# Optimization experiments

Measured on AMD Instinct MI355X. Metric: run time of the kernel, lower is better.

The kernel has to match this reference:

```python
import jax, jax.numpy as jnp
import numpy as np

HID, DIN, ORDER = 64, 1, 2
EPS = 1e-5


def conv1x1(x, W, b):
    # x: [b, c_in, n] -> [b, c_out, n]
    return jnp.einsum('oi,bin->bon', W, x) + b[:, None]


def gconv(x, supports, W, b, order, include_self):
    outs = [x] if include_self else []
    for A in supports:
        x1 = jnp.einsum('bcv,wv->bcw', x, A)
        outs.append(x1)
        for _ in range(order - 1):
            x1 = jnp.einsum('bcv,wv->bcw', x1, A)
            outs.append(x1)
    return conv1x1(jnp.concatenate(outs, axis=1), W, b)


def _forward(x, mask, adj, h0, fs_W, fs_b, li_W, li_b, gc_W, gc_b, lo_W, lo_b,
             ro_W, ro_b, prelu_a, f_W, f_b, u_W, u_b, c_W, c_b, gn_g, gn_beta):
    B = x.shape[0]
    supports = [adj[0], adj[1]]
    h = jnp.broadcast_to(h0, (B,) + h0.shape)  # [b, HID, n]

    def step(h, inp):
        x_s, m_s = inp  # [b, DIN, n] each
        mbool = m_s > 0
        # first stage prediction from hidden state
        xs_hat_1 = conv1x1(h, fs_W, fs_b)
        x1 = jnp.where(mbool, x_s, xs_hat_1)
        # spatial decoder (order=1, no attention)
        x_in = conv1x1(jnp.concatenate([x1, m_s, h], axis=1), li_W, li_b)
        out = gconv(x_in, supports, gc_W, gc_b, order=1, include_self=False)
        out = conv1x1(jnp.concatenate([out, h], axis=1), lo_W, lo_b)
        out = jnp.where(out >= 0, out, prelu_a * out)  # PReLU
        repr_s = jnp.concatenate([out, h], axis=1)     # [b, 2*HID, n]
        xs_hat_2 = conv1x1(repr_s, ro_W, ro_b)
        x2 = jnp.where(mbool, x1, xs_hat_2)
        # GCGRU cell (order-2 graph conv gates, include_self=True)
        rnn_in = jnp.concatenate([x2, m_s], axis=1)    # [b, 2*DIN, n]
        xh = jnp.concatenate([rnn_in, h], axis=1)
        r = jax.nn.sigmoid(gconv(xh, supports, f_W, f_b, ORDER, True))
        u = jax.nn.sigmoid(gconv(xh, supports, u_W, u_b, ORDER, True))
        xc = jnp.concatenate([rnn_in, r * h], axis=1)
        c = jnp.tanh(gconv(xc, supports, c_W, c_b, ORDER, True))
        h_new = u * h + (1.0 - u) * c
        # GroupNorm(num_groups=1): normalize over (C, N) per sample
        mu = h_new.mean(axis=(1, 2), keepdims=True)
        var = h_new.var(axis=(1, 2), keepdims=True)
        h_n = (h_new - mu) / jnp.sqrt(var + EPS) * gn_g[:, None] + gn_beta[:, None]
        return h_n, (xs_hat_2, xs_hat_1, h_n, repr_s)

    xs = jnp.moveaxis(x, -1, 0)     # [T, b, DIN, n]
    ms = jnp.moveaxis(mask, -1, 0)
    _, (imp, pred, states, reprs) = jax.lax.scan(step, h, (xs, ms))
    imputations = jnp.moveaxis(imp, 0, -1)          # [b, DIN, n, T]
    predictions = jnp.moveaxis(pred, 0, -1)
    states = jnp.moveaxis(states, 0, -1)[None]      # [n_layers=1, b, HID, n, T]
    representations = jnp.moveaxis(reprs, 0, -1)    # [b, 2*HID, n, T]
    return imputations, predictions, representations, states


def setup_inputs() -> dict:
    key = jax.random.key(0)
    ks = jax.random.split(key, 24)
    B, N, T = 8, 1024, 24
    rnn_in = 2 * DIN                 # x + mask
    dec_in = rnn_in + HID            # 66
    gate_in = 5 * (rnn_in + HID)     # (order*support_len + self) * (d_in + hidden)

    def w(k, o, i):
        return (jax.random.normal(k, (o, i), jnp.float32) / np.sqrt(i)).astype(jnp.float32)

    x = jax.random.normal(ks[0], (B, DIN, N, T), jnp.float32)
    mask = jax.random.bernoulli(ks[1], 0.8, (B, DIN, N, T)).astype(jnp.float32)
    A = jax.random.uniform(ks[2], (N, N), jnp.float32)
    A = A * (A > 0.97)  # sparse-ish graph
    fwd = A / (A.sum(1, keepdims=True) + 1e-8)
    bwd = A.T / (A.T.sum(1, keepdims=True) + 1e-8)
    adj = jnp.stack([fwd, bwd])
    return {
        'x': x, 'mask': mask, 'adj': adj,
        'h0': jax.random.normal(ks[3], (HID, N), jnp.float32) / np.sqrt(HID),
        'fs_W': w(ks[4], DIN, HID), 'fs_b': jnp.zeros((DIN,), jnp.float32),
        'li_W': w(ks[5], HID, dec_in), 'li_b': jnp.zeros((HID,), jnp.float32),
        'gc_W': w(ks[6], HID, 2 * HID), 'gc_b': jnp.zeros((HID,), jnp.float32),
        'lo_W': w(ks[7], HID, 2 * HID), 'lo_b': jnp.zeros((HID,), jnp.float32),
        'ro_W': w(ks[8], DIN, 2 * HID), 'ro_b': jnp.zeros((DIN,), jnp.float32),
        'prelu_a': jnp.float32(0.25),
        'f_W': w(ks[9], HID, gate_in), 'f_b': jnp.zeros((HID,), jnp.float32),
        'u_W': w(ks[10], HID, gate_in), 'u_b': jnp.zeros((HID,), jnp.float32),
        'c_W': w(ks[11], HID, gate_in), 'c_b': jnp.zeros((HID,), jnp.float32),
        'gn_g': jnp.ones((HID,), jnp.float32), 'gn_beta': jnp.zeros((HID,), jnp.float32),
    }


def reference(x, mask, adj, h0, fs_W, fs_b, li_W, li_b, gc_W, gc_b, lo_W, lo_b,
              ro_W, ro_b, prelu_a, f_W, f_b, u_W, u_b, c_W, c_b, gn_g, gn_beta):
    return _forward(x, mask, adj, h0, fs_W, fs_b, li_W, li_b, gc_W, gc_b,
                    lo_W, lo_b, ro_W, ro_b, prelu_a, f_W, f_b, u_W, u_b,
                    c_W, c_b, gn_g, gn_beta)
```

## Files before the change

### kernel.cpp

```cpp
#include <hip/hip_runtime.h>
#include <hip/hip_bf16.h>

typedef __hip_bfloat16 bf16;

constexpr int NV=1024, TT=24, BB=8, CAP=80;

constexpr int O_CVAL = 0;
constexpr int O_CIDX = 163840;
constexpr int O_CCNT = 327680;
constexpr int O_LIWT = 329728;
constexpr int O_GCWT = 333952;
constexpr int O_LOWT = 342144;
constexpr int O_FWT  = 350336;
constexpr int O_UWT  = 371456;
constexpr int O_CWT  = 392576;
constexpr int O_H    = 413696;
constexpr int O_T1   = 937984;
constexpr int O_T3   = 1986560;
constexpr int O_XH   = 2510848;
constexpr int O_Z1F  = 3067904;
constexpr int O_Z1B  = 3624960;
constexpr int O_PART = 4182016;
constexpr int O_RST  = 5296144;
constexpr int O_SST  = 17879056;
constexpr size_t WS_FLOATS = 24170512;
constexpr int O_XC = O_T1;
constexpr int O_U  = O_T3;

constexpr int OFF_IMP  = 0;
constexpr int OFF_PRED = 196608;
constexpr int OFF_REPR = 393216;
constexpr int OFF_ST   = 25559040;

__device__ __forceinline__ bf16 f2b(float v){ return __float2bfloat16(v); }
__device__ __forceinline__ float b2f(bf16 v){ return __bfloat162float(v); }

__global__ __launch_bounds__(64) void k_csr(const float* __restrict__ adj, float* __restrict__ ws){
  int row = blockIdx.x, lane = threadIdx.x;
  const float* a = adj + (size_t)row*NV;
  float* val = ws + O_CVAL + (size_t)row*CAP;
  int* idx = (int*)(ws+O_CIDX) + (size_t)row*CAP;
  int count = 0;
  for(int ch=0; ch<NV/64; ++ch){
    float v = a[ch*64+lane];
    unsigned long long m = __ballot(v != 0.f);
    int pre = __popcll(m & ((1ull<<lane)-1ull));
    if(v != 0.f){ int p = count+pre; if(p<CAP){ idx[p]=ch*64+lane; val[p]=v; } }
    count += __popcll(m);
  }
  if(lane==0) ((int*)(ws+O_CCNT))[row] = count>CAP?CAP:count;
}

__global__ void k_prep_wt(const float* __restrict__ liW, const float* __restrict__ gcW,
    const float* __restrict__ loW, const float* __restrict__ fW,
    const float* __restrict__ uW, const float* __restrict__ cW, float* __restrict__ ws){
  int g = blockIdx.x*blockDim.x + threadIdx.x, G = gridDim.x*blockDim.x;
  for(int i=g;i<66*64;i+=G){ int k=i>>6, c=i&63; ws[O_LIWT+i]=liW[c*66+k]; }
  for(int i=g;i<128*64;i+=G){ int k=i>>6, c=i&63; ws[O_GCWT+i]=gcW[c*128+k]; ws[O_LOWT+i]=loW[c*128+k]; }
  for(int i=g;i<330*64;i+=G){ int k=i>>6, c=i&63; ws[O_FWT+i]=fW[c*330+k]; ws[O_UWT+i]=uW[c*330+k]; ws[O_CWT+i]=cW[c*330+k]; }
}

__global__ __launch_bounds__(256) void k_h0(const float* __restrict__ h0, float* __restrict__ ws){
  int g = blockIdx.x*blockDim.x + threadIdx.x;
  if(g >= BB*NV*64) return;
  int c = g&63, n = (g>>6)&1023;
  ws[O_H + g] = h0[c*NV + n];
}

__global__ __launch_bounds__(256) void kA(float* __restrict__ ws,
    const float* __restrict__ x, const float* __restrict__ mask,
    const float* __restrict__ fsW, const float* __restrict__ fsb,
    const float* __restrict__ lib, const float* __restrict__ gng,
    const float* __restrict__ gnb, float* __restrict__ dout, int t){
  __shared__ float hs[4][2][64];
  __shared__ float musd[8][2];
  int tid = threadIdx.x, wid = tid>>6, lane = tid&63;
  int n = blockIdx.x;
  if(t > 0){
    const float2* part = (const float2*)(ws+O_PART);
    int b = wid*2 + (lane>>5);
    int l5 = lane&31;
    float sx=0.f, sq=0.f;
    for(int i=l5;i<1024;i+=32){ float2 pp = part[b*1024+i]; sx+=pp.x; sq+=pp.y; }
    #pragma unroll
    for(int off=16;off;off>>=1){ sx+=__shfl_xor(sx,off,64); sq+=__shfl_xor(sq,off,64); }
    if(l5==0){ float mu=sx*(1.f/65536.f);
               musd[b][0]=mu; musd[b][1]=rsqrtf(sq*(1.f/65536.f)-mu*mu+1e-5f); }
    __syncthreads();
  }
  float gg = gng[lane], gb = gnb[lane];
  float x1v[2], xmv[2];
  #pragma unroll
  for(int j=0;j<2;++j){
    int b = wid*2+j;
    size_t col = (size_t)(b*NV+n);
    float h = ws[O_H + col*64 + lane];
    if(t > 0){
      h = (h - musd[b][0])*musd[b][1]*gg + gb;
      ws[O_H + col*64 + lane] = h;
      ((bf16*)(ws+O_SST))[(size_t)(t-1)*(BB*NV*64) + col*64 + lane] = f2b(h);
    }
    hs[wid][j][lane] = h;
    float pv = fsW[lane]*h;
    #pragma unroll
    for(int off=32; off; off>>=1) pv += __shfl_xor(pv, off, 64);
    float pred = pv + fsb[0];
    float xm = mask[col*TT + t];
    x1v[j] = (xm>0.f) ? x[col*TT + t] : pred;
    xmv[j] = xm;
    if(lane==0) dout[OFF_PRED + col*TT + t] = pred;
  }
  const float* Wt = ws + O_LIWT;
  float lb = lib[lane];
  float w0 = Wt[lane], w1 = Wt[64+lane];
  float a0 = lb + w0*x1v[0] + w1*xmv[0];
  float a1 = lb + w0*x1v[1] + w1*xmv[1];
  for(int j=0;j<64;++j){
    float w = Wt[(2+j)*64+lane];
    a0 += w*hs[wid][0][j];
    a1 += w*hs[wid][1][j];
  }
  ws[O_T1 + (size_t)((wid*2  )*NV+n)*64 + lane] = a0;
  ws[O_T1 + (size_t)((wid*2+1)*NV+n)*64 + lane] = a1;
}

__global__ __launch_bounds__(256) void kB(float* __restrict__ ws,
    const float* __restrict__ x, const float* __restrict__ mask,
    const float* __restrict__ gcb, const float* __restrict__ lob,
    const float* __restrict__ prelu, const float* __restrict__ roW,
    const float* __restrict__ rob, float* __restrict__ dout, int t){
  __shared__ float pq[4][2][128];
  int tid=threadIdx.x, wid=tid>>6, lane=tid&63;
  int n = blockIdx.x;
  int b0 = wid*2, b1 = wid*2+1;
  const int* ccnt = (const int*)(ws+O_CCNT);
  float p0=0.f,p1=0.f,q0=0.f,q1=0.f;
  {
    int cn = ccnt[n];
    const int* id = (const int*)(ws+O_CIDX) + (size_t)n*CAP;
    const float* vl = ws + O_CVAL + (size_t)n*CAP;
    #pragma unroll 4
    for(int k=0;k<cn;++k){
      float a = vl[k]; int ix = id[k];
      p0 += a*ws[O_T1 + (size_t)(b0*NV+ix)*64 + lane];
      p1 += a*ws[O_T1 + (size_t)(b1*NV+ix)*64 + lane];
    }
  }
  {
    int cn = ccnt[NV+n];
    const int* id = (const int*)(ws+O_CIDX) + (size_t)(NV+n)*CAP;
    const float* vl = ws + O_CVAL + (size_t)(NV+n)*CAP;
    #pragma unroll 4
    for(int k=0;k<cn;++k){
      float a = vl[k]; int ix = id[k];
      q0 += a*ws[O_T1 + (size_t)(b0*NV+ix)*64 + lane];
      q1 += a*ws[O_T1 + (size_t)(b1*NV+ix)*64 + lane];
    }
  }
  pq[wid][0][lane]=p0; pq[wid][0][64+lane]=q0;
  pq[wid][1][lane]=p1; pq[wid][1][64+lane]=q1;
  const float* Gt = ws + O_GCWT;
  float g0 = gcb[lane], g1 = g0;
  for(int j=0;j<128;++j){
    float w = Gt[j*64+lane];
    g0 += w*pq[wid][0][j];
    g1 += w*pq[wid][1][j];
  }
  float hv0 = ws[O_H + (size_t)(b0*NV+n)*64 + lane];
  float hv1 = ws[O_H + (size_t)(b1*NV+n)*64 + lane];
  pq[wid][0][lane]=g0; pq[wid][0][64+lane]=hv0;
  pq[wid][1][lane]=g1; pq[wid][1][64+lane]=hv1;
  const float* Lt = ws + O_LOWT;
  float o0 = lob[lane], o1 = o0;
  for(int j=0;j<128;++j){
    float w = Lt[j*64+lane];
    o0 += w*pq[wid][0][j];
    o1 += w*pq[wid][1][j];
  }
  float a = prelu[0];
  float r0 = roW[lane], r1 = roW[64+lane], rb0 = rob[0];
  bf16* reprs = (bf16*)(ws + O_RST);
  #pragma unroll
  for(int j=0;j<2;++j){
    int b = wid*2+j;
    float ov = (j? o1 : o0);
    float hv = (j? hv1 : hv0);
    ov = (ov>=0.f)? ov : a*ov;
    size_t col = (size_t)(b*NV+n);
    size_t rbo = (((size_t)t*BB + b)*NV + n)*128;
    reprs[rbo + lane]      = f2b(ov);
    reprs[rbo + 64 + lane] = f2b(hv);
    float rv = r0*ov + r1*hv;
    #pragma unroll
    for(int off=32; off; off>>=1) rv += __shfl_xor(rv, off, 64);
    float xs2 = rv + rb0;
    float xm = mask[col*TT+t];
    float x2 = (xm>0.f) ? x[col*TT+t] : xs2;
    if(lane==0) dout[OFF_IMP + col*TT + t] = xs2;
    float* xh = ws + O_XH + col*68;
    xh[2+lane] = hv;
    if(lane==0){ xh[0]=x2; xh[1]=xm; }
  }
}

__global__ __launch_bounds__(256) void k_prop(float* __restrict__ ws, int srcF, int srcB,
    int dstF, int dstB){
  int tid=threadIdx.x, wid = tid>>6, lane = tid&63;
  int n = blockIdx.x;
  int b0 = wid*2, b1 = wid*2+1;
  const int* ccnt = (const int*)(ws+O_CCNT);
  bool hi = lane < 2;
  {
    int cn = ccnt[n];
    const int* id = (const int*)(ws+O_CIDX) + (size_t)n*CAP;
    const float* vl = ws + O_CVAL + (size_t)n*CAP;
    float a00=0.f,a01=0.f,a10=0.f,a11=0.f;
    #pragma unroll 4
    for(int k=0;k<cn;++k){
      float a = vl[k]; int ix = id[k];
      const float* r0 = ws + srcF + (size_t)(b0*NV + ix)*68;
      const float* r1 = ws + srcF + (size_t)(b1*NV + ix)*68;
      a00 += a*r0[lane]; if(hi) a01 += a*r0[64+lane];
      a10 += a*r1[lane]; if(hi) a11 += a*r1[64+lane];
    }
    float* d0 = ws + dstF + (size_t)(b0*NV+n)*68;
    float* d1 = ws + dstF + (size_t)(b1*NV+n)*68;
    d0[lane]=a00; if(hi) d0[64+lane]=a01;
    d1[lane]=a10; if(hi) d1[64+lane]=a11;
  }
  {
    int cn = ccnt[NV+n];
    const int* id = (const int*)(ws+O_CIDX) + (size_t)(NV+n)*CAP;
    const float* vl = ws + O_CVAL + (size_t)(NV+n)*CAP;
    float a00=0.f,a01=0.f,a10=0.f,a11=0.f;
    #pragma unroll 4
    for(int k=0;k<cn;++k){
      float a = vl[k]; int ix = id[k];
      const float* r0 = ws + srcB + (size_t)(b0*NV + ix)*68;
      const float* r1 = ws + srcB + (size_t)(b1*NV + ix)*68;
      a00 += a*r0[lane]; if(hi) a01 += a*r0[64+lane];
      a10 += a*r1[lane]; if(hi) a11 += a*r1[64+lane];
    }
    float* d0 = ws + dstB + (size_t)(b0*NV+n)*68;
    float* d1 = ws + dstB + (size_t)(b1*NV+n)*68;
    d0[lane]=a00; if(hi) d0[64+lane]=a01;
    d1[lane]=a10; if(hi) d1[64+lane]=a11;
  }
}

__global__ __launch_bounds__(512) void kD(float* __restrict__ ws,
    const float* __restrict__ fb, const float* __restrict__ ub){
  __shared__ float vec[4][2][332];
  __shared__ float acc[8][4][64];
  int tid=threadIdx.x, w=tid>>6, lane=tid&63;
  int pair=w>>1, half=w&1;
  int n = blockIdx.x;
  int b0 = pair*2, b1 = b0+1;
  size_t c0=(size_t)(b0*NV+n), c1=(size_t)(b1*NV+n);
  const int* ccnt = (const int*)(ws+O_CCNT);
  bool hi = lane < 2;
  if(half==0){
    const float* xh0 = ws + O_XH + c0*68;
    const float* xh1 = ws + O_XH + c1*68;
    const float* z1f0 = ws + O_Z1F + c0*68;
    const float* z1f1 = ws + O_Z1F + c1*68;
    vec[pair][0][lane]=xh0[lane];     if(hi) vec[pair][0][64+lane]=xh0[64+lane];
    vec[pair][1][lane]=xh1[lane];     if(hi) vec[pair][1][64+lane]=xh1[64+lane];
    vec[pair][0][66+lane]=z1f0[lane]; if(hi) vec[pair][0][130+lane]=z1f0[64+lane];
    vec[pair][1][66+lane]=z1f1[lane]; if(hi) vec[pair][1][130+lane]=z1f1[64+lane];
    int cn = ccnt[n];
    const int* id = (const int*)(ws+O_CIDX) + (size_t)n*CAP;
    const float* vl = ws + O_CVAL + (size_t)n*CAP;
    float a00=0.f,a01=0.f,a10=0.f,a11=0.f;
    #pragma unroll 4
    for(int k=0;k<cn;++k){
      float a = vl[k]; int ix = id[k];
      const float* r0 = ws + O_Z1F + (size_t)(b0*NV+ix)*68;
      const float* r1 = ws + O_Z1F + (size_t)(b1*NV+ix)*68;
      a00 += a*r0[lane]; if(hi) a01 += a*r0[64+lane];
      a10 += a*r1[lane]; if(hi) a11 += a*r1[64+lane];
    }
    vec[pair][0][132+lane]=a00; if(hi) vec[pair][0][196+lane]=a01;
    vec[pair][1][132+lane]=a10; if(hi) vec[pair][1][196+lane]=a11;
  } else {
    const float* z1b0 = ws + O_Z1B + c0*68;
    const float* z1b1 = ws + O_Z1B + c1*68;
    vec[pair][0][198+lane]=z1b0[lane]; if(hi) vec[pair][0][262+lane]=z1b0[64+lane];
    vec[pair][1][198+lane]=z1b1[lane]; if(hi) vec[pair][1][262+lane]=z1b1[64+lane];
    int cn = ccnt[NV+n];
    const int* id = (const int*)(ws+O_CIDX) + (size_t)(NV+n)*CAP;
    const float* vl = ws + O_CVAL + (size_t)(NV+n)*CAP;
    float a00=0.f,a01=0.f,a10=0.f,a11=0.f;
    #pragma unroll 4
    for(int k=0;k<cn;++k){
      float a = vl[k]; int ix = id[k];
      const float* r0 = ws + O_Z1B + (size_t)(b0*NV+ix)*68;
      const float* r1 = ws + O_Z1B + (size_t)(b1*NV+ix)*68;
      a00 += a*r0[lane]; if(hi) a01 += a*r0[64+lane];
      a10 += a*r1[lane]; if(hi) a11 += a*r1[64+lane];
    }
    vec[pair][0][264+lane]=a00; if(hi) vec[pair][0][328+lane]=a01;
    vec[pair][1][264+lane]=a10; if(hi) vec[pair][1][328+lane]=a11;
  }
  __syncthreads();
  const float* Ft = ws + O_FWT;
  const float* Ut = ws + O_UWT;
  int k0 = half*165, k1 = k0+165;
  float ar0 = half? 0.f : fb[lane];
  float au0 = half? 0.f : ub[lane];
  float ar1 = ar0, au1 = au0;
  for(int k=k0;k<k1;++k){
    float wf = Ft[k*64+lane];
    float wu = Ut[k*64+lane];
    float v0 = vec[pair][0][k], v1 = vec[pair][1][k];
    ar0 += wf*v0; ar1 += wf*v1;
    au0 += wu*v0; au1 += wu*v1;
  }
  acc[w][0][lane]=ar0; acc[w][1][lane]=ar1; acc[w][2][lane]=au0; acc[w][3][lane]=au1;
  __syncthreads();
  if(half==0){
    ar0 += acc[w+1][0][lane]; ar1 += acc[w+1][1][lane];
    au0 += acc[w+1][2][lane]; au1 += acc[w+1][3][lane];
    float r0 = 1.f/(1.f+expf(-ar0)), r1v = 1.f/(1.f+expf(-ar1));
    float u0 = 1.f/(1.f+expf(-au0)), u1v = 1.f/(1.f+expf(-au1));
    float hv0 = ws[O_H + c0*64 + lane];
    float hv1 = ws[O_H + c1*64 + lane];
    ws[O_U + c0*64 + lane] = u0;
    ws[O_U + c1*64 + lane] = u1v;
    float* xc0 = ws + O_XC + c0*68;
    float* xc1 = ws + O_XC + c1*68;
    xc0[2+lane] = r0*hv0; xc1[2+lane] = r1v*hv1;
    if(hi){ xc0[lane] = vec[pair][0][lane]; xc1[lane] = vec[pair][1][lane]; }
  }
}

__global__ __launch_bounds__(512) void kF(float* __restrict__ ws, const float* __restrict__ cb){
  __shared__ float vec[4][2][332];
  __shared__ float acc[8][2][64];
  int tid=threadIdx.x, w=tid>>6, lane=tid&63;
  int pair=w>>1, half=w&1;
  int n = blockIdx.x;
  int b0 = pair*2, b1 = b0+1;
  size_t c0=(size_t)(b0*NV+n), c1=(size_t)(b1*NV+n);
  const int* ccnt = (const int*)(ws+O_CCNT);
  bool hi = lane < 2;
  if(half==0){
    const float* xc0 = ws + O_XC + c0*68;
    const float* xc1 = ws + O_XC + c1*68;
    const float* w1f0 = ws + O_Z1F + c0*68;
    const float* w1f1 = ws + O_Z1F + c1*68;
    vec[pair][0][lane]=xc0[lane];      if(hi) vec[pair][0][64+lane]=xc0[64+lane];
    vec[pair][1][lane]=xc1[lane];      if(hi) vec[pair][1][64+lane]=xc1[64+lane];
    vec[pair][0][66+lane]=w1f0[lane];  if(hi) vec[pair][0][130+lane]=w1f0[64+lane];
    vec[pair][1][66+lane]=w1f1[lane];  if(hi) vec[pair][1][130+lane]=w1f1[64+lane];
    int cn = ccnt[n];
    const int* id = (const int*)(ws+O_CIDX) + (size_t)n*CAP;
    const float* vl = ws + O_CVAL + (size_t)n*CAP;
    float a00=0.f,a01=0.f,a10=0.f,a11=0.f;
    #pragma unroll 4
    for(int k=0;k<cn;++k){
      float a = vl[k]; int ix = id[k];
      const float* r0 = ws + O_Z1F + (size_t)(b0*NV+ix)*68;
      const float* r1 = ws + O_Z1F + (size_t)(b1*NV+ix)*68;
      a00 += a*r0[lane]; if(hi) a01 += a*r0[64+lane];
      a10 += a*r1[lane]; if(hi) a11 += a*r1[64+lane];
    }
    vec[pair][0][132+lane]=a00; if(hi) vec[pair][0][196+lane]=a01;
    vec[pair][1][132+lane]=a10; if(hi) vec[pair][1][196+lane]=a11;
  } else {
    const float* w1b0 = ws + O_Z1B + c0*68;
    const float* w1b1 = ws + O_Z1B + c1*68;
    vec[pair][0][198+lane]=w1b0[lane]; if(hi) vec[pair][0][262+lane]=w1b0[64+lane];
    vec[pair][1][198+lane]=w1b1[lane]; if(hi) vec[pair][1][262+lane]=w1b1[64+lane];
    int cn = ccnt[NV+n];
    const int* id = (const int*)(ws+O_CIDX) + (size_t)(NV+n)*CAP;
    const float* vl = ws + O_CVAL + (size_t)(NV+n)*CAP;
    float a00=0.f,a01=0.f,a10=0.f,a11=0.f;
    #pragma unroll 4
    for(int k=0;k<cn;++k){
      float a = vl[k]; int ix = id[k];
      const float* r0 = ws + O_Z1B + (size_t)(b0*NV+ix)*68;
      const float* r1 = ws + O_Z1B + (size_t)(b1*NV+ix)*68;
      a00 += a*r0[lane]; if(hi) a01 += a*r0[64+lane];
      a10 += a*r1[lane]; if(hi) a11 += a*r1[64+lane];
    }
    vec[pair][0][264+lane]=a00; if(hi) vec[pair][0][328+lane]=a01;
    vec[pair][1][264+lane]=a10; if(hi) vec[pair][1][328+lane]=a11;
  }
  __syncthreads();
  const float* Ct = ws + O_CWT;
  int k0 = half*165, k1 = k0+165;
  float ac0 = half? 0.f : cb[lane];
  float ac1 = ac0;
  for(int k=k0;k<k1;++k){
    float wc = Ct[k*64+lane];
    ac0 += wc*vec[pair][0][k];
    ac1 += wc*vec[pair][1][k];
  }
  acc[w][0][lane]=ac0; acc[w][1][lane]=ac1;
  __syncthreads();
  if(half==0){
    ac0 += acc[w+1][0][lane];
    ac1 += acc[w+1][1][lane];
    #pragma unroll
    for(int j=0;j<2;++j){
      int b = b0+j;
      size_t col = (j? c1 : c0);
      float cd = tanhf(j? ac1 : ac0);
      float hv = ws[O_H + col*64 + lane];
      float u  = ws[O_U + col*64 + lane];
      float hn = u*hv + (1.f-u)*cd;
      ws[O_H + col*64 + lane] = hn;
      float s = hn, sq = hn*hn;
      #pragma unroll
      for(int off=32; off; off>>=1){ s += __shfl_xor(s, off, 64); sq += __shfl_xor(sq, off, 64); }
      if(lane==0) ((float2*)(ws+O_PART))[b*1024 + n] = make_float2(s, sq);
    }
  }
}

__global__ __launch_bounds__(256) void k_final(float* __restrict__ ws,
    const float* __restrict__ gng, const float* __restrict__ gnb){
  __shared__ float musd[8][2];
  int tid=threadIdx.x, wid=tid>>6, lane=tid&63;
  int n = blockIdx.x;
  const float2* part = (const float2*)(ws+O_PART);
  {
    int b = wid*2 + (lane>>5);
    int l5 = lane&31;
    float sx=0.f, sq=0.f;
    for(int i=l5;i<1024;i+=32){ float2 pp = part[b*1024+i]; sx+=pp.x; sq+=pp.y; }
    #pragma unroll
    for(int off=16;off;off>>=1){ sx+=__shfl_xor(sx,off,64); sq+=__shfl_xor(sq,off,64); }
    if(l5==0){ float mu=sx*(1.f/65536.f);
               musd[b][0]=mu; musd[b][1]=rsqrtf(sq*(1.f/65536.f)-mu*mu+1e-5f); }
    __syncthreads();
  }
  float gg=gng[lane], gb=gnb[lane];
  #pragma unroll
  for(int j=0;j<2;++j){
    int b = wid*2+j;
    size_t col = (size_t)(b*NV+n);
    float hn = ws[O_H + col*64 + lane];
    float h = (hn-musd[b][0])*musd[b][1]*gg + gb;
    ((bf16*)(ws+O_SST))[(size_t)23*(BB*NV*64) + col*64 + lane] = f2b(h);
  }
}

__global__ __launch_bounds__(256) void k_transpose(const float* __restrict__ ws, float* __restrict__ dout,
                                                   int srcOff, int dstOff, int CH){
  __shared__ bf16 ld[32][16][26];
  int ct = CH/16;
  int per_b = 32*ct;
  int b = blockIdx.x / per_b;
  int r = blockIdx.x - b*per_b;
  int n0 = (r/ct)*32, ch0 = (r - (r/ct)*ct)*16;
  const bf16* src = (const bf16*)(ws + srcOff);
  for(int t=0;t<TT;++t){
    for(int i=threadIdx.x;i<512;i+=256){
      int cc=i&15, nn=i>>4;
      ld[nn][cc][t] = src[(((size_t)t*BB + b)*NV + n0+nn)*CH + ch0+cc];
    }
  }
  __syncthreads();
  for(int i=threadIdx.x;i<512;i+=256){
    int nn=i&31, cc=i>>5;
    size_t ob = ((size_t)(b*CH + ch0+cc)*NV + n0+nn)*TT;
    #pragma unroll
    for(int t=0;t<TT;++t) dout[dstOff + ob + t] = b2f(ld[nn][cc][t]);
  }
}

extern "C" void kernel_launch(void* const* d_in, const int* in_sizes, int n_in,
                              void* d_out, int out_size, void* d_ws, size_t ws_size,
                              hipStream_t stream){
  if(ws_size < WS_FLOATS * sizeof(float)) return;
  if(n_in < 23) return;

  float* ws = (float*)d_ws;
  float* out = (float*)d_out;

  const float* x    = (const float*)d_in[0];
  const float* mask = (const float*)d_in[1];
  const float* adj  = (const float*)d_in[2];
  const float* h0   = (const float*)d_in[3];
  const float* fsW  = (const float*)d_in[4];
  const float* fsb  = (const float*)d_in[5];
  const float* lib  = (const float*)d_in[7];
  const float* gcb  = (const float*)d_in[9];
  const float* lob  = (const float*)d_in[11];
  const float* roW  = (const float*)d_in[12];
  const float* rob  = (const float*)d_in[13];
  const float* prelu= (const float*)d_in[14];
  const float* fb   = (const float*)d_in[16];
  const float* ub   = (const float*)d_in[18];
  const float* cb   = (const float*)d_in[20];
  const float* gng  = (const float*)d_in[21];
  const float* gnb  = (const float*)d_in[22];

  k_csr    <<<dim3(2048), dim3(64),  0, stream>>>(adj, ws);
  k_prep_wt<<<dim3(64),   dim3(256), 0, stream>>>(
      (const float*)d_in[6], (const float*)d_in[8], (const float*)d_in[10],
      (const float*)d_in[15], (const float*)d_in[17], (const float*)d_in[19], ws);
  k_h0     <<<dim3(2048), dim3(256), 0, stream>>>(h0, ws);

  for(int t=0; t<TT; ++t){
    kA    <<<dim3(1024), dim3(256), 0, stream>>>(ws, x, mask, fsW, fsb, lib, gng, gnb, out, t);
    kB    <<<dim3(1024), dim3(256), 0, stream>>>(ws, x, mask, gcb, lob, prelu, roW, rob, out, t);
    k_prop<<<dim3(1024), dim3(256), 0, stream>>>(ws, O_XH, O_XH, O_Z1F, O_Z1B);
    kD    <<<dim3(1024), dim3(512), 0, stream>>>(ws, fb, ub);
    k_prop<<<dim3(1024), dim3(256), 0, stream>>>(ws, O_XC, O_XC, O_Z1F, O_Z1B);
    kF    <<<dim3(1024), dim3(512), 0, stream>>>(ws, cb);
  }
  k_final<<<dim3(1024), dim3(256), 0, stream>>>(ws, gng, gnb);

  k_transpose<<<dim3(2048), dim3(256), 0, stream>>>(ws, out, O_RST, OFF_REPR, 128);
  k_transpose<<<dim3(1024), dim3(256), 0, stream>>>(ws, out, O_SST, OFF_ST, 64);
}
```

Baseline: 5.158 ms.

## Pack gate weights as bf16 pairs and process four batches per wave

Weight matrices for the graph-conv and gate 1x1 convs are stored as packed bf16 pairs, which halves weight-load traffic in kB, kD and kF. kD and kF are also restructured so each wave handles four batch columns instead of two, with two nodes per block and half the grid. This reuses each loaded weight across more batches. It costs precision on the weights and raises register and LDS use per block, which may lower occupancy.

```diff
diff --git a/kernel.cpp b/kernel.cpp
--- a/kernel.cpp
+++ b/kernel.cpp
@@ -2,6 +2,7 @@
 #include <hip/hip_bf16.h>
 
 typedef __hip_bfloat16 bf16;
+typedef unsigned int uint32;
 
 constexpr int NV=1024, TT=24, BB=8, CAP=80;
 
@@ -35,6 +36,14 @@
 __device__ __forceinline__ bf16 f2b(float v){ return __float2bfloat16(v); }
 __device__ __forceinline__ float b2f(bf16 v){ return __bfloat162float(v); }
 
+__device__ __forceinline__ uint32 pkbf(float f){
+  uint32 u = __float_as_uint(f);
+  return (u + 0x7fffu + ((u>>16)&1u)) >> 16;
+}
+__device__ __forceinline__ uint32 pk2(float lo, float hi){ return pkbf(lo) | (pkbf(hi)<<16); }
+__device__ __forceinline__ float unplo(uint32 u){ return __uint_as_float(u<<16); }
+__device__ __forceinline__ float unphi(uint32 u){ return __uint_as_float(u & 0xffff0000u); }
+
 __global__ __launch_bounds__(64) void k_csr(const float* __restrict__ adj, float* __restrict__ ws){
   int row = blockIdx.x, lane = threadIdx.x;
   const float* a = adj + (size_t)row*NV;
@@ -56,8 +65,17 @@
     const float* __restrict__ uW, const float* __restrict__ cW, float* __restrict__ ws){
   int g = blockIdx.x*blockDim.x + threadIdx.x, G = gridDim.x*blockDim.x;
   for(int i=g;i<66*64;i+=G){ int k=i>>6, c=i&63; ws[O_LIWT+i]=liW[c*66+k]; }
-  for(int i=g;i<128*64;i+=G){ int k=i>>6, c=i&63; ws[O_GCWT+i]=gcW[c*128+k]; ws[O_LOWT+i]=loW[c*128+k]; }
-  for(int i=g;i<330*64;i+=G){ int k=i>>6, c=i&63; ws[O_FWT+i]=fW[c*330+k]; ws[O_UWT+i]=uW[c*330+k]; ws[O_CWT+i]=cW[c*330+k]; }
+  for(int i=g;i<64*64;i+=G){
+    int p=i>>6, c=i&63;
+    ((uint32*)(ws+O_GCWT))[i] = pk2(gcW[c*128+2*p], gcW[c*128+2*p+1]);
+    ((uint32*)(ws+O_LOWT))[i] = pk2(loW[c*128+2*p], loW[c*128+2*p+1]);
+  }
+  for(int i=g;i<165*64;i+=G){
+    int p=i>>6, c=i&63;
+    ((uint32*)(ws+O_FWT))[i] = pk2(fW[c*330+2*p], fW[c*330+2*p+1]);
+    ((uint32*)(ws+O_UWT))[i] = pk2(uW[c*330+2*p], uW[c*330+2*p+1]);
+    ((uint32*)(ws+O_CWT))[i] = pk2(cW[c*330+2*p], cW[c*330+2*p+1]);
+  }
 }
 
 __global__ __launch_bounds__(256) void k_h0(const float* __restrict__ h0, float* __restrict__ ws){
@@ -159,23 +177,25 @@
   }
   pq[wid][0][lane]=p0; pq[wid][0][64+lane]=q0;
   pq[wid][1][lane]=p1; pq[wid][1][64+lane]=q1;
-  const float* Gt = ws + O_GCWT;
+  const uint32* Gt = (const uint32*)(ws + O_GCWT);
   float g0 = gcb[lane], g1 = g0;
-  for(int j=0;j<128;++j){
-    float w = Gt[j*64+lane];
-    g0 += w*pq[wid][0][j];
-    g1 += w*pq[wid][1][j];
+  for(int p=0;p<64;++p){
+    uint32 u = Gt[p*64+lane];
+    float wl = unplo(u), wh = unphi(u);
+    g0 += wl*pq[wid][0][2*p] + wh*pq[wid][0][2*p+1];
+    g1 += wl*pq[wid][1][2*p] + wh*pq[wid][1][2*p+1];
   }
   float hv0 = ws[O_H + (size_t)(b0*NV+n)*64 + lane];
   float hv1 = ws[O_H + (size_t)(b1*NV+n)*64 + lane];
   pq[wid][0][lane]=g0; pq[wid][0][64+lane]=hv0;
   pq[wid][1][lane]=g1; pq[wid][1][64+lane]=hv1;
-  const float* Lt = ws + O_LOWT;
+  const uint32* Lt = (const uint32*)(ws + O_LOWT);
   float o0 = lob[lane], o1 = o0;
-  for(int j=0;j<128;++j){
-    float w = Lt[j*64+lane];
-    o0 += w*pq[wid][0][j];
-    o1 += w*pq[wid][1][j];
+  for(int p=0;p<64;++p){
+    uint32 u = Lt[p*64+lane];
+    float wl = unplo(u), wh = unphi(u);
+    o0 += wl*pq[wid][0][2*p] + wh*pq[wid][0][2*p+1];
+    o1 += wl*pq[wid][1][2*p] + wh*pq[wid][1][2*p+1];
   }
   float a = prelu[0];
   float r0 = roW[lane], r1 = roW[64+lane], rb0 = rob[0];
@@ -250,163 +270,183 @@
 
 __global__ __launch_bounds__(512) void kD(float* __restrict__ ws,
     const float* __restrict__ fb, const float* __restrict__ ub){
-  __shared__ float vec[4][2][332];
-  __shared__ float acc[8][4][64];
+  __shared__ float vec[4][4][332];
+  __shared__ float acc[8][8][64];
   int tid=threadIdx.x, w=tid>>6, lane=tid&63;
-  int pair=w>>1, half=w&1;
-  int n = blockIdx.x;
-  int b0 = pair*2, b1 = b0+1;
-  size_t c0=(size_t)(b0*NV+n), c1=(size_t)(b1*NV+n);
+  int quad=w>>1, half=w&1;
+  int n = blockIdx.x*2 + (quad>>1);
+  int bg = (quad&1)*4;
   const int* ccnt = (const int*)(ws+O_CCNT);
   bool hi = lane < 2;
   if(half==0){
-    const float* xh0 = ws + O_XH + c0*68;
-    const float* xh1 = ws + O_XH + c1*68;
-    const float* z1f0 = ws + O_Z1F + c0*68;
-    const float* z1f1 = ws + O_Z1F + c1*68;
-    vec[pair][0][lane]=xh0[lane];     if(hi) vec[pair][0][64+lane]=xh0[64+lane];
-    vec[pair][1][lane]=xh1[lane];     if(hi) vec[pair][1][64+lane]=xh1[64+lane];
-    vec[pair][0][66+lane]=z1f0[lane]; if(hi) vec[pair][0][130+lane]=z1f0[64+lane];
-    vec[pair][1][66+lane]=z1f1[lane]; if(hi) vec[pair][1][130+lane]=z1f1[64+lane];
-    int cn = ccnt[n];
-    const int* id = (const int*)(ws+O_CIDX) + (size_t)n*CAP;
-    const float* vl = ws + O_CVAL + (size_t)n*CAP;
-    float a00=0.f,a01=0.f,a10=0.f,a11=0.f;
-    #pragma unroll 4
-    for(int k=0;k<cn;++k){
-      float a = vl[k]; int ix = id[k];
-      const float* r0 = ws + O_Z1F + (size_t)(b0*NV+ix)*68;
-      const float* r1 = ws + O_Z1F + (size_t)(b1*NV+ix)*68;
-      a00 += a*r0[lane]; if(hi) a01 += a*r0[64+lane];
-      a10 += a*r1[lane]; if(hi) a11 += a*r1[64+lane];
-    }
-    vec[pair][0][132+lane]=a00; if(hi) vec[pair][0][196+lane]=a01;
-    vec[pair][1][132+lane]=a10; if(hi) vec[pair][1][196+lane]=a11;
+    #pragma unroll
+    for(int j=0;j<4;++j){
+      size_t c = (size_t)((bg+j)*NV+n);
+      const float* xh = ws+O_XH+c*68;
+      const float* zf = ws+O_Z1F+c*68;
+      vec[quad][j][lane]=xh[lane];    if(hi) vec[quad][j][64+lane]=xh[64+lane];
+      vec[quad][j][66+lane]=zf[lane]; if(hi) vec[quad][j][130+lane]=zf[64+lane];
+    }
+    int cn=ccnt[n];
+    const int* id=(const int*)(ws+O_CIDX)+(size_t)n*CAP;
+    const float* vl=ws+O_CVAL+(size_t)n*CAP;
+    float a0[4]={0,0,0,0}, a1[4]={0,0,0,0};
+    #pragma unroll 2
+    for(int k=0;k<cn;++k){
+      float a=vl[k]; int ix=id[k];
+      #pragma unroll
+      for(int j=0;j<4;++j){
+        const float* r = ws+O_Z1F+(size_t)((bg+j)*NV+ix)*68;
+        a0[j]+=a*r[lane]; if(hi) a1[j]+=a*r[64+lane];
+      }
+    }
+    #pragma unroll
+    for(int j=0;j<4;++j){ vec[quad][j][132+lane]=a0[j]; if(hi) vec[quad][j][196+lane]=a1[j]; }
   } else {
-    const float* z1b0 = ws + O_Z1B + c0*68;
-    const float* z1b1 = ws + O_Z1B + c1*68;
-    vec[pair][0][198+lane]=z1b0[lane]; if(hi) vec[pair][0][262+lane]=z1b0[64+lane];
-    vec[pair][1][198+lane]=z1b1[lane]; if(hi) vec[pair][1][262+lane]=z1b1[64+lane];
-    int cn = ccnt[NV+n];
-    const int* id = (const int*)(ws+O_CIDX) + (size_t)(NV+n)*CAP;
-    const float* vl = ws + O_CVAL + (size_t)(NV+n)*CAP;
-    float a00=0.f,a01=0.f,a10=0.f,a11=0.f;
-    #pragma unroll 4
-    for(int k=0;k<cn;++k){
-      float a = vl[k]; int ix = id[k];
-      const float* r0 = ws + O_Z1B + (size_t)(b0*NV+ix)*68;
-      const float* r1 = ws + O_Z1B + (size_t)(b1*NV+ix)*68;
-      a00 += a*r0[lane]; if(hi) a01 += a*r0[64+lane];
-      a10 += a*r1[lane]; if(hi) a11 += a*r1[64+lane];
-    }
-    vec[pair][0][264+lane]=a00; if(hi) vec[pair][0][328+lane]=a01;
-    vec[pair][1][264+lane]=a10; if(hi) vec[pair][1][328+lane]=a11;
+    #pragma unroll
+    for(int j=0;j<4;++j){
+      size_t c = (size_t)((bg+j)*NV+n);
+      const float* zb = ws+O_Z1B+c*68;
+      vec[quad][j][198+lane]=zb[lane]; if(hi) vec[quad][j][262+lane]=zb[64+lane];
+    }
+    int cn=ccnt[NV+n];
+    const int* id=(const int*)(ws+O_CIDX)+(size_t)(NV+n)*CAP;
+    const float* vl=ws+O_CVAL+(size_t)(NV+n)*CAP;
+    float a0[4]={0,0,0,0}, a1[4]={0,0,0,0};
+    #pragma unroll 2
+    for(int k=0;k<cn;++k){
+      float a=vl[k]; int ix=id[k];
+      #pragma unroll
+      for(int j=0;j<4;++j){
+        const float* r = ws+O_Z1B+(size_t)((bg+j)*NV+ix)*68;
+        a0[j]+=a*r[lane]; if(hi) a1[j]+=a*r[64+lane];
+      }
+    }
+    #pragma unroll
+    for(int j=0;j<4;++j){ vec[quad][j][264+lane]=a0[j]; if(hi) vec[quad][j][328+lane]=a1[j]; }
   }
   __syncthreads();
-  const float* Ft = ws + O_FWT;
-  const float* Ut = ws + O_UWT;
-  int k0 = half*165, k1 = k0+165;
-  float ar0 = half? 0.f : fb[lane];
-  float au0 = half? 0.f : ub[lane];
-  float ar1 = ar0, au1 = au0;
-  for(int k=k0;k<k1;++k){
-    float wf = Ft[k*64+lane];
-    float wu = Ut[k*64+lane];
-    float v0 = vec[pair][0][k], v1 = vec[pair][1][k];
-    ar0 += wf*v0; ar1 += wf*v1;
-    au0 += wu*v0; au1 += wu*v1;
-  }
-  acc[w][0][lane]=ar0; acc[w][1][lane]=ar1; acc[w][2][lane]=au0; acc[w][3][lane]=au1;
+  const uint32* F2 = (const uint32*)(ws+O_FWT);
+  const uint32* U2 = (const uint32*)(ws+O_UWT);
+  int p0 = half? 83 : 0, p1 = half? 165 : 83;
+  float ar[4], au[4];
+  float fbi = half? 0.f : fb[lane];
+  float ubi = half? 0.f : ub[lane];
+  #pragma unroll
+  for(int j=0;j<4;++j){ ar[j]=fbi; au[j]=ubi; }
+  for(int p=p0;p<p1;++p){
+    uint32 uf = F2[p*64+lane];
+    uint32 uu = U2[p*64+lane];
+    float fl=unplo(uf), fh=unphi(uf);
+    float ul=unplo(uu), uh=unphi(uu);
+    #pragma unroll
+    for(int j=0;j<4;++j){
+      float v0 = vec[quad][j][2*p], v1 = vec[quad][j][2*p+1];
+      ar[j] += fl*v0 + fh*v1;
+      au[j] += ul*v0 + uh*v1;
+    }
+  }
+  #pragma unroll
+  for(int j=0;j<4;++j){ acc[w][j][lane]=ar[j]; acc[w][4+j][lane]=au[j]; }
   __syncthreads();
   if(half==0){
-    ar0 += acc[w+1][0][lane]; ar1 += acc[w+1][1][lane];
-    au0 += acc[w+1][2][lane]; au1 += acc[w+1][3][lane];
-    float r0 = 1.f/(1.f+expf(-ar0)), r1v = 1.f/(1.f+expf(-ar1));
-    float u0 = 1.f/(1.f+expf(-au0)), u1v = 1.f/(1.f+expf(-au1));
-    float hv0 = ws[O_H + c0*64 + lane];
-    float hv1 = ws[O_H + c1*64 + lane];
-    ws[O_U + c0*64 + lane] = u0;
-    ws[O_U + c1*64 + lane] = u1v;
-    float* xc0 = ws + O_XC + c0*68;
-    float* xc1 = ws + O_XC + c1*68;
-    xc0[2+lane] = r0*hv0; xc1[2+lane] = r1v*hv1;
-    if(hi){ xc0[lane] = vec[pair][0][lane]; xc1[lane] = vec[pair][1][lane]; }
+    #pragma unroll
+    for(int j=0;j<4;++j){
+      float arj = ar[j] + acc[w+1][j][lane];
+      float auj = au[j] + acc[w+1][4+j][lane];
+      float r = 1.f/(1.f+expf(-arj));
+      float u = 1.f/(1.f+expf(-auj));
+      size_t col = (size_t)((bg+j)*NV+n);
+      float hv = ws[O_H + col*64 + lane];
+      ws[O_U + col*64 + lane] = u;
+      float* xc = ws + O_XC + col*68;
+      xc[2+lane] = r*hv;
+      if(hi) xc[lane] = vec[quad][j][lane];
+    }
   }
 }
 
 __global__ __launch_bounds__(512) void kF(float* __restrict__ ws, const float* __restrict__ cb){
-  __shared__ float vec[4][2][332];
-  __shared__ float acc[8][2][64];
+  __shared__ float vec[4][4][332];
+  __shared__ float acc[8][4][64];
   int tid=threadIdx.x, w=tid>>6, lane=tid&63;
-  int pair=w>>1, half=w&1;
-  int n = blockIdx.x;
-  int b0 = pair*2, b1 = b0+1;
-  size_t c0=(size_t)(b0*NV+n), c1=(size_t)(b1*NV+n);
+  int quad=w>>1, half=w&1;
+  int n = blockIdx.x*2 + (quad>>1);
+  int bg = (quad&1)*4;
   const int* ccnt = (const int*)(ws+O_CCNT);
   bool hi = lane < 2;
   if(half==0){
-    const float* xc0 = ws + O_XC + c0*68;
-    const float* xc1 = ws + O_XC + c1*68;
-    const float* w1f0 = ws + O_Z1F + c0*68;
-    const float* w1f1 = ws + O_Z1F + c1*68;
-    vec[pair][0][lane]=xc0[lane];      if(hi) vec[pair][0][64+lane]=xc0[64+lane];
-    vec[pair][1][lane]=xc1[lane];      if(hi) vec[pair][1][64+lane]=xc1[64+lane];
-    vec[pair][0][66+lane]=w1f0[lane];  if(hi) vec[pair][0][130+lane]=w1f0[64+lane];
-    vec[pair][1][66+lane]=w1f1[lane];  if(hi) vec[pair][1][130+lane]=w1f1[64+lane];
-    int cn = ccnt[n];
-    const int* id = (const int*)(ws+O_CIDX) + (size_t)n*CAP;
-    const float* vl = ws + O_CVAL + (size_t)n*CAP;
-    float a00=0.f,a01=0.f,a10=0.f,a11=0.f;
-    #pragma unroll 4
-    for(int k=0;k<cn;++k){
-      float a = vl[k]; int ix = id[k];
-      const float* r0 = ws + O_Z1F + (size_t)(b0*NV+ix)*68;
-      const float* r1 = ws + O_Z1F + (size_t)(b1*NV+ix)*68;
-      a00 += a*r0[lane]; if(hi) a01 += a*r0[64+lane];
-      a10 += a*r1[lane]; if(hi) a11 += a*r1[64+lane];
-    }
-    vec[pair][0][132+lane]=a00; if(hi) vec[pair][0][196+lane]=a01;
-    vec[pair][1][132+lane]=a10; if(hi) vec[pair][1][196+lane]=a11;
+    #pragma unroll
+    for(int j=0;j<4;++j){
+      size_t c = (size_t)((bg+j)*NV+n);
+      const float* xc = ws+O_XC+c*68;
+      const float* wf = ws+O_Z1F+c*68;
+      vec[quad][j][lane]=xc[lane];    if(hi) vec[quad][j][64+lane]=xc[64+lane];
+      vec[quad][j][66+lane]=wf[lane]; if(hi) vec[quad][j][130+lane]=wf[64+lane];
+    }
+    int cn=ccnt[n];
+    const int* id=(const int*)(ws+O_CIDX)+(size_t)n*CAP;
+    const float* vl=ws+O_CVAL+(size_t)n*CAP;
+    float a0[4]={0,0,0,0}, a1[4]={0,0,0,0};
+    #pragma unroll 2
+    for(int k=0;k<cn;++k){
+      float a=vl[k]; int ix=id[k];
+      #pragma unroll
+      for(int j=0;j<4;++j){
+        const float* r = ws+O_Z1F+(size_t)((bg+j)*NV+ix)*68;
+        a0[j]+=a*r[lane]; if(hi) a1[j]+=a*r[64+lane];
+      }
+    }
+    #pragma unroll
+    for(int j=0;j<4;++j){ vec[quad][j][132+lane]=a0[j]; if(hi) vec[quad][j][196+lane]=a1[j]; }
   } else {
-    const float* w1b0 = ws + O_Z1B + c0*68;
-    const float* w1b1 = ws + O_Z1B + c1*68;
-    vec[pair][0][198+lane]=w1b0[lane]; if(hi) vec[pair][0][262+lane]=w1b0[64+lane];
-    vec[pair][1][198+lane]=w1b1[lane]; if(hi) vec[pair][1][262+lane]=w1b1[64+lane];
-    int cn = ccnt[NV+n];
-    const int* id = (const int*)(ws+O_CIDX) + (size_t)(NV+n)*CAP;
-    const float* vl = ws + O_CVAL + (size_t)(NV+n)*CAP;
-    float a00=0.f,a01=0.f,a10=0.f,a11=0.f;
-    #pragma unroll 4
-    for(int k=0;k<cn;++k){
-      float a = vl[k]; int ix = id[k];
-      const float* r0 = ws + O_Z1B + (size_t)(b0*NV+ix)*68;
-      const float* r1 = ws + O_Z1B + (size_t)(b1*NV+ix)*68;
-      a00 += a*r0[lane]; if(hi) a01 += a*r0[64+lane];
-      a10 += a*r1[lane]; if(hi) a11 += a*r1[64+lane];
-    }
-    vec[pair][0][264+lane]=a00; if(hi) vec[pair][0][328+lane]=a01;
-    vec[pair][1][264+lane]=a10; if(hi) vec[pair][1][328+lane]=a11;
+    #pragma unroll
+    for(int j=0;j<4;++j){
+      size_t c = (size_t)((bg+j)*NV+n);
+      const float* wb = ws+O_Z1B+c*68;
+      vec[quad][j][198+lane]=wb[lane]; if(hi) vec[quad][j][262+lane]=wb[64+lane];
+    }
+    int cn=ccnt[NV+n];
+    const int* id=(const int*)(ws+O_CIDX)+(size_t)(NV+n)*CAP;
+    const float* vl=ws+O_CVAL+(size_t)(NV+n)*CAP;
+    float a0[4]={0,0,0,0}, a1[4]={0,0,0,0};
+    #pragma unroll 2
+    for(int k=0;k<cn;++k){
+      float a=vl[k]; int ix=id[k];
+      #pragma unroll
+      for(int j=0;j<4;++j){
+        const float* r = ws+O_Z1B+(size_t)((bg+j)*NV+ix)*68;
+        a0[j]+=a*r[lane]; if(hi) a1[j]+=a*r[64+lane];
+      }
+    }
+    #pragma unroll
+    for(int j=0;j<4;++j){ vec[quad][j][264+lane]=a0[j]; if(hi) vec[quad][j][328+lane]=a1[j]; }
   }
   __syncthreads();
-  const float* Ct = ws + O_CWT;
-  int k0 = half*165, k1 = k0+165;
-  float ac0 = half? 0.f : cb[lane];
-  float ac1 = ac0;
-  for(int k=k0;k<k1;++k){
-    float wc = Ct[k*64+lane];
-    ac0 += wc*vec[pair][0][k];
-    ac1 += wc*vec[pair][1][k];
-  }
-  acc[w][0][lane]=ac0; acc[w][1][lane]=ac1;
+  const uint32* C2 = (const uint32*)(ws+O_CWT);
+  int p0 = half? 83 : 0, p1 = half? 165 : 83;
+  float ac[4];
+  float cbi = half? 0.f : cb[lane];
+  #pragma unroll
+  for(int j=0;j<4;++j) ac[j]=cbi;
+  for(int p=p0;p<p1;++p){
+    uint32 uc = C2[p*64+lane];
+    float cl=unplo(uc), ch=unphi(uc);
+    #pragma unroll
+    for(int j=0;j<4;++j){
+      float v0 = vec[quad][j][2*p], v1 = vec[quad][j][2*p+1];
+      ac[j] += cl*v0 + ch*v1;
+    }
+  }
+  #pragma unroll
+  for(int j=0;j<4;++j) acc[w][j][lane]=ac[j];
   __syncthreads();
   if(half==0){
-    ac0 += acc[w+1][0][lane];
-    ac1 += acc[w+1][1][lane];
-    #pragma unroll
-    for(int j=0;j<2;++j){
-      int b = b0+j;
-      size_t col = (j? c1 : c0);
-      float cd = tanhf(j? ac1 : ac0);
+    #pragma unroll
+    for(int j=0;j<4;++j){
+      float acj = ac[j] + acc[w+1][j][lane];
+      float cd = tanhf(acj);
+      size_t col = (size_t)((bg+j)*NV+n);
       float hv = ws[O_H + col*64 + lane];
       float u  = ws[O_U + col*64 + lane];
       float hn = u*hv + (1.f-u)*cd;
@@ -414,7 +454,7 @@
       float s = hn, sq = hn*hn;
       #pragma unroll
       for(int off=32; off; off>>=1){ s += __shfl_xor(s, off, 64); sq += __shfl_xor(sq, off, 64); }
-      if(lane==0) ((float2*)(ws+O_PART))[b*1024 + n] = make_float2(s, sq);
+      if(lane==0) ((float2*)(ws+O_PART))[(bg+j)*1024 + n] = make_float2(s, sq);
     }
   }
 }
@@ -508,9 +548,9 @@
     kA    <<<dim3(1024), dim3(256), 0, stream>>>(ws, x, mask, fsW, fsb, lib, gng, gnb, out, t);
     kB    <<<dim3(1024), dim3(256), 0, stream>>>(ws, x, mask, gcb, lob, prelu, roW, rob, out, t);
     k_prop<<<dim3(1024), dim3(256), 0, stream>>>(ws, O_XH, O_XH, O_Z1F, O_Z1B);
-    kD    <<<dim3(1024), dim3(512), 0, stream>>>(ws, fb, ub);
+    kD    <<<dim3(512),  dim3(512), 0, stream>>>(ws, fb, ub);
     k_prop<<<dim3(1024), dim3(256), 0, stream>>>(ws, O_XC, O_XC, O_Z1F, O_Z1B);
-    kF    <<<dim3(1024), dim3(512), 0, stream>>>(ws, cb);
+    kF    <<<dim3(512),  dim3(512), 0, stream>>>(ws, cb);
   }
   k_final<<<dim3(1024), dim3(256), 0, stream>>>(ws, gng, gnb);
 
```

Measured after the change: 6.306 ms. 22.2% more time.
